# Optimization experiments

Measured on AMD Instinct MI355X. Metric: run time of the kernel, lower is better.

The kernel has to match this reference:

```python
import jax, jax.numpy as jnp
import numpy as np

K = 3       # kernel_size
RATE = 2    # dilation rate
NH = 8      # num_heads
EPS = 1e-5  # InstanceNorm eps


def _conv1x1(x, W, b):
    # x: [B,C,H,W], W: [O,C], b: [O]
    return jnp.einsum('bchw,oc->bohw', x, W) + b[None, :, None, None]


def _inorm(x):
    mu = jnp.mean(x, axis=(2, 3), keepdims=True)
    var = jnp.var(x, axis=(2, 3), keepdims=True)
    return (x - mu) / jnp.sqrt(var + EPS)


def _extract_patches(x):
    # dilated KxK patches, stride 1, 'same' grid -> [B, C, K*K, H, W]
    B, C, H, W = x.shape
    pad = RATE * (K - 1) // 2
    xp = jnp.pad(x, ((0, 0), (0, 0), (pad, pad), (pad, pad)))
    taps = [xp[:, :, i * RATE:i * RATE + H, j * RATE:j * RATE + W]
            for i in range(K) for j in range(K)]
    return jnp.stack(taps, axis=2)


def setup_inputs() -> dict:
    key = jax.random.key(0)
    ks = jax.random.split(key, 8)
    B, C, H, W, A = 1, 64, 64, 64, 128
    features = jax.random.normal(ks[0], (B, C, H, W), jnp.float32)
    masks = jax.random.uniform(ks[1], (B, 1, H, W), jnp.float32)
    s_in = 1.0 / np.sqrt(C).astype(np.float32)
    Wq = jax.random.normal(ks[2], (A, C), jnp.float32) * s_in
    bq = jnp.zeros((A,), jnp.float32)
    Wk = jax.random.normal(ks[3], (A, C), jnp.float32) * s_in
    bk = jnp.zeros((A,), jnp.float32)
    Wo = jax.random.normal(ks[4], (C, C), jnp.float32) * s_in
    bo = jnp.zeros((C,), jnp.float32)
    return dict(features=features, masks=masks, Wq=Wq, bq=bq,
                Wk=Wk, bk=bk, Wo=Wo, bo=bo)


def reference(features, masks, Wq, bq, Wk, bk, Wo, bo):
    B, C, H, W = features.shape
    A = Wq.shape[0]
    hc = A // NH
    L = H * W
    KK = K * K

    m = (masks > 0.5).astype(features.dtype)          # 1 = hole
    f_masked = features * m
    f_unmasked = features * (1.0 - m)

    q = jax.nn.relu(_inorm(_conv1x1(f_masked, Wq, bq)))    # [B,A,H,W]
    k = jax.nn.relu(_inorm(_conv1x1(f_unmasked, Wk, bk)))  # [B,A,H,W]

    # per-head dilated patch banks: [B,NH,hc*KK,L]
    qp = _extract_patches(q).reshape(B, NH, hc * KK, L)
    kp = _extract_patches(k).reshape(B, NH, hc * KK, L)

    # patch-correlation attention per head: [B,NH,L,L]
    attn = jax.nn.softmax(jnp.einsum('bndq,bndk->bnqk', qp, kp), axis=-1)

    # value patch bank from unmasked features: [B,C*KK,L]
    vp = _extract_patches(f_unmasked).reshape(B, C * KK, L)

    # sample value patches: [B,NH,L,C*KK]
    sampled = jnp.einsum('bnqk,bdk->bnqd', attn, vp)

    # fold: average the KK taps per channel, then average over heads
    attended = sampled.reshape(B, NH, L, C, KK).mean(axis=4).mean(axis=1)  # [B,L,C]
    attended = attended.transpose(0, 2, 1).reshape(B, C, H, W)

    return jax.nn.relu(_inorm(_conv1x1(attended, Wo, bo)))
```

## Files before the change

kernel.cpp:

```cpp
#include <hip/hip_runtime.h>
#include <hip/hip_bf16.h>


#define LL 4096
#define CC 64
#define AA 128
#define NH_ 8
#define KSTR 144
#define LOG2E 1.44269504088896340736f

typedef _Float16 half8 __attribute__((ext_vector_type(8)));
typedef float floatx4 __attribute__((ext_vector_type(4)));
typedef int intx4 __attribute__((ext_vector_type(4)));

__device__ __forceinline__ float fexp2(float x) {
    float r;
    asm("v_exp_f32 %0, %1" : "=v"(r) : "v"(x));
    return r;
}

__global__ __launch_bounds__(512) void prep_kernel(
    const float* __restrict__ feat,
    const float* __restrict__ masks,
    const float* __restrict__ Wq, const float* __restrict__ bq,
    const float* __restrict__ Wk, const float* __restrict__ bk,
    _Float16* __restrict__ q_act, _Float16* __restrict__ k_act,
    _Float16* __restrict__ vb)
{
    const int tid = threadIdx.x;
    const int b = blockIdx.x;
    __shared__ float sW[CC];
    __shared__ float sm[16];

    if (b >= 2 * AA) {
        int c = b - 2 * AA;
        for (int p = 0; p < 8; ++p) {
            int l = p * 512 + tid;
            int y = l >> 6, x = l & 63;
            float s = 0.f;
            for (int ty = 0; ty < 3; ++ty) {
                int yy = y + 2 * (ty - 1);
                if (yy < 0 || yy > 63) continue;
                for (int tx = 0; tx < 3; ++tx) {
                    int xx = x + 2 * (tx - 1);
                    if (xx < 0 || xx > 63) continue;
                    int ll = yy * 64 + xx;
                    float hole = masks[ll] > 0.5f ? 1.f : 0.f;
                    s += feat[c * LL + ll] * (1.f - hole);
                }
            }
            vb[c * LL + l] = (_Float16)(s * (1.f / 9.f));
        }
        return;
    }

    const int a = b & (AA - 1);
    const int sel = b >> 7;
    const float* Wrow = (sel ? Wk : Wq) + a * CC;
    const float bias = sel ? bk[a] : bq[a];
    if (tid < CC) sW[tid] = Wrow[tid];
    __syncthreads();

    float acc[8];
#pragma unroll
    for (int p = 0; p < 8; ++p) acc[p] = 0.f;
    for (int c = 0; c < CC; ++c) {
        float wc = sW[c];
        const float* fr = feat + (size_t)c * LL + tid;
#pragma unroll
        for (int p = 0; p < 8; ++p) acc[p] += wc * fr[p * 512];
    }

    float vals[8];
    float s1 = 0.f, s2 = 0.f;
#pragma unroll
    for (int p = 0; p < 8; ++p) {
        int l = p * 512 + tid;
        float hole = masks[l] > 0.5f ? 1.f : 0.f;
        float mf = sel ? (1.f - hole) : hole;
        float v = acc[p] * mf + bias;
        vals[p] = v; s1 += v; s2 += v * v;
    }
    for (int off = 32; off; off >>= 1) {
        s1 += __shfl_down(s1, off, 64);
        s2 += __shfl_down(s2, off, 64);
    }
    int wv = tid >> 6, ln = tid & 63;
    if (ln == 0) { sm[wv * 2] = s1; sm[wv * 2 + 1] = s2; }
    __syncthreads();
    s1 = 0.f; s2 = 0.f;
#pragma unroll
    for (int i = 0; i < 8; ++i) { s1 += sm[2 * i]; s2 += sm[2 * i + 1]; }
    float mu = s1 * (1.f / LL);
    float inv = rsqrtf(s2 * (1.f / LL) - mu * mu + 1e-5f);

    const float oscale = sel ? 1.f : LOG2E;
    _Float16* act = (sel ? k_act : q_act) + (size_t)a * LL;
#pragma unroll
    for (int p = 0; p < 8; ++p) {
        int l = p * 512 + tid;
        float v = (vals[p] - mu) * inv;
        act[l] = (_Float16)(v > 0.f ? v * oscale : 0.f);
    }
}

__global__ __launch_bounds__(256) void build_kp(
    const _Float16* __restrict__ k_act, _Float16* __restrict__ kp)
{
    const int n = blockIdx.x, y = blockIdx.y;
    const int tid = threadIdx.x;
    const _Float16* ka = k_act + (size_t)n * 16 * LL;
    __shared__ _Float16 kt[16][3][72];

    for (int idx = tid; idx < 16 * 3 * 68; idx += 256) {
        int row = idx / 68, xr = idx - row * 68;
        int ah = row / 3, ty = row - ah * 3;
        int yy = y + 2 * (ty - 1);
        int xx = xr - 2;
        _Float16 v = (_Float16)0.f;
        if (yy >= 0 && yy <= 63 && xx >= 0 && xx <= 63)
            v = ka[ah * LL + yy * 64 + xx];
        kt[ah][ty][xr] = v;
    }
    __syncthreads();

    _Float16* base = kp + ((size_t)n * LL + y * 64) * KSTR;
#pragma unroll
    for (int i = 0; i < 5; ++i) {
        int idx = tid + i * 256;
        if (idx < 64 * 18) {
            int x = idx / 18, c18 = idx - x * 18;
            half8 v8;
#pragma unroll
            for (int j = 0; j < 8; ++j) {
                int d = c18 * 8 + j;
                int ah = d / 9, t = d - ah * 9;
                int ty = t / 3, tx = t - ty * 3;
                v8[j] = kt[ah][ty][x + 2 * tx];
            }
            *(half8*)(base + (size_t)idx * 8) = v8;
        }
    }
}

__global__ __launch_bounds__(256, 2) void attn_kernel(
    const _Float16* __restrict__ q_act, const _Float16* __restrict__ kp,
    const _Float16* __restrict__ vb,
    _Float16* __restrict__ Opart, float* __restrict__ ml)
{
    const int bid = blockIdx.x;
    const int n = bid & 7;
    const int slot = bid >> 3;
    const int qt2 = slot & 31;
    const int h = slot >> 5;
    const int jt0 = h * 32;
    const int tid = threadIdx.x;
    const int w = tid >> 6, lane = tid & 63;
    const int l15 = lane & 15, quad = lane >> 4;

    __shared__ __align__(16) _Float16 Bk[2][64 * KSTR + 16];

    if (tid < 32) Bk[tid >> 4][64 * KSTR + (tid & 15)] = (_Float16)0.f;

    const _Float16* kpn = kp + (size_t)n * LL * KSTR;

    auto issue_bk = [&](int jt, _Float16* dst) {
        const char* tile = (const char*)(kpn + (size_t)jt * 64 * KSTR) + (lane << 4);
        for (int c = w; c < 18; c += 4) {
            __builtin_amdgcn_global_load_lds(
                (const __attribute__((address_space(1))) void*)(tile + c * 1024),
                (__attribute__((address_space(3))) void*)(dst + c * 512),
                16, 0, 0);
        }
    };

    half8 afrag[2][5];
    {
        const _Float16* qa = q_act + (size_t)n * 16 * LL;
        const int x = w * 16 + l15;
#pragma unroll
        for (int rs = 0; rs < 2; ++rs) {
            const int y = qt2 * 2 + rs;
#pragma unroll
            for (int ks = 0; ks < 5; ++ks) {
#pragma unroll
                for (int j = 0; j < 8; ++j) {
                    int d = ks * 32 + quad * 8 + j;
                    _Float16 v = (_Float16)0.f;
                    if (d < 144) {
                        int ah = d / 9, t = d - ah * 9;
                        int ty = t / 3, tx = t - ty * 3;
                        int yy = y + 2 * (ty - 1);
                        int xx = x + 2 * (tx - 1);
                        if (yy >= 0 && yy <= 63 && xx >= 0 && xx <= 63)
                            v = qa[ah * LL + yy * 64 + xx];
                    }
                    afrag[rs][ks][j] = v;
                }
            }
        }
    }

    floatx4 accO[2][4];
    float mrow[2], lrow[2];
#pragma unroll
    for (int rs = 0; rs < 2; ++rs) {
        mrow[rs] = -1e30f; lrow[rs] = 0.f;
#pragma unroll
        for (int i = 0; i < 4; ++i) accO[rs][i] = (floatx4){0.f, 0.f, 0.f, 0.f};
    }

    const int aLo = (((quad & 1) << 5) + l15) << 2;
    const int aHi = aLo + 64;
    const bool selHi = (quad >> 1) != 0;

    const _Float16* vpl = vb + (size_t)l15 * LL + quad * 8;

    issue_bk(jt0, Bk[0]);

    int cur = 0;
    for (int it = 0; it < 32; ++it) {
        __syncthreads();

        if (it < 31) issue_bk(jt0 + it + 1, Bk[cur ^ 1]);

        const _Float16* vp = vpl + (jt0 + it) * 64;
        half8 vfrag[4][2];
#pragma unroll
        for (int nt = 0; nt < 4; ++nt)
#pragma unroll
            for (int ks2 = 0; ks2 < 2; ++ks2)
                vfrag[nt][ks2] = *(const half8*)(vp + (size_t)nt * 16 * LL + ks2 * 32);

        const _Float16* bk = Bk[cur];

        floatx4 accS[2][4];
#pragma unroll
        for (int rs = 0; rs < 2; ++rs)
#pragma unroll
            for (int i = 0; i < 4; ++i) accS[rs][i] = (floatx4){0.f, 0.f, 0.f, 0.f};
        __builtin_amdgcn_s_setprio(1);
        for (int ks = 0; ks < 5; ++ks) {
#pragma unroll
            for (int nt = 0; nt < 4; ++nt) {
                half8 bfr = *(const half8*)(bk + (nt * 16 + l15) * KSTR + ks * 32 + quad * 8);
                accS[0][nt] = __builtin_amdgcn_mfma_f32_16x16x32_f16(bfr, afrag[0][ks], accS[0][nt], 0, 0, 0);
                accS[1][nt] = __builtin_amdgcn_mfma_f32_16x16x32_f16(bfr, afrag[1][ks], accS[1][nt], 0, 0, 0);
            }
        }
        __builtin_amdgcn_s_setprio(0);

        half8 pfr[2][2];
#pragma unroll
        for (int rs = 0; rs < 2; ++rs) {
            float t0 = fmaxf(fmaxf(accS[rs][0][0], accS[rs][0][1]), fmaxf(accS[rs][0][2], accS[rs][0][3]));
            float t1 = fmaxf(fmaxf(accS[rs][1][0], accS[rs][1][1]), fmaxf(accS[rs][1][2], accS[rs][1][3]));
            float t2 = fmaxf(fmaxf(accS[rs][2][0], accS[rs][2][1]), fmaxf(accS[rs][2][2], accS[rs][2][3]));
            float t3 = fmaxf(fmaxf(accS[rs][3][0], accS[rs][3][1]), fmaxf(accS[rs][3][2], accS[rs][3][3]));
            float tm = fmaxf(fmaxf(t0, t1), fmaxf(t2, t3));
            if (!__all(tm <= mrow[rs] + 3.0f)) {
                tm = fmaxf(tm, __shfl_xor(tm, 16, 64));
                tm = fmaxf(tm, __shfl_xor(tm, 32, 64));
                float mn = fmaxf(mrow[rs], tm);
                float alpha = fexp2(mrow[rs] - mn);
                mrow[rs] = mn;
                lrow[rs] *= alpha;
                float af[4];
#pragma unroll
                for (int r = 0; r < 4; ++r) af[r] = __shfl(alpha, quad * 4 + r, 16);
#pragma unroll
                for (int nt = 0; nt < 4; ++nt)
#pragma unroll
                    for (int r = 0; r < 4; ++r) accO[rs][nt][r] *= af[r];
            }
            float rsum = 0.f;
#pragma unroll
            for (int nt = 0; nt < 4; ++nt)
#pragma unroll
                for (int r = 0; r < 4; ++r) {
                    float pv = fexp2(accS[rs][nt][r] - mrow[rs]);
                    accS[rs][nt][r] = pv;
                    rsum += pv;
                }
            lrow[rs] += rsum;

            int pkw[4][2];
#pragma unroll
            for (int nt = 0; nt < 4; ++nt)
#pragma unroll
                for (int rp = 0; rp < 2; ++rp) {
                    auto hp = __builtin_amdgcn_cvt_pkrtz(accS[rs][nt][2 * rp],
                                                         accS[rs][nt][2 * rp + 1]);
                    pkw[nt][rp] = __builtin_bit_cast(int, hp);
                }
#pragma unroll
            for (int ks2 = 0; ks2 < 2; ++ks2) {
                int w0A = __builtin_amdgcn_ds_bpermute(aLo, pkw[2 * ks2][0]);
                int w0B = __builtin_amdgcn_ds_bpermute(aLo, pkw[2 * ks2 + 1][0]);
                int w1A = __builtin_amdgcn_ds_bpermute(aLo, pkw[2 * ks2][1]);
                int w1B = __builtin_amdgcn_ds_bpermute(aLo, pkw[2 * ks2 + 1][1]);
                int w2A = __builtin_amdgcn_ds_bpermute(aHi, pkw[2 * ks2][0]);
                int w2B = __builtin_amdgcn_ds_bpermute(aHi, pkw[2 * ks2 + 1][0]);
                int w3A = __builtin_amdgcn_ds_bpermute(aHi, pkw[2 * ks2][1]);
                int w3B = __builtin_amdgcn_ds_bpermute(aHi, pkw[2 * ks2 + 1][1]);
                intx4 wvv;
                wvv[0] = selHi ? w0B : w0A;
                wvv[1] = selHi ? w1B : w1A;
                wvv[2] = selHi ? w2B : w2A;
                wvv[3] = selHi ? w3B : w3A;
                pfr[rs][ks2] = __builtin_bit_cast(half8, wvv);
            }
        }

        __builtin_amdgcn_s_setprio(1);
#pragma unroll
        for (int ks2 = 0; ks2 < 2; ++ks2) {
#pragma unroll
            for (int nt = 0; nt < 4; ++nt) {
                accO[0][nt] = __builtin_amdgcn_mfma_f32_16x16x32_f16(pfr[0][ks2], vfrag[nt][ks2], accO[0][nt], 0, 0, 0);
                accO[1][nt] = __builtin_amdgcn_mfma_f32_16x16x32_f16(pfr[1][ks2], vfrag[nt][ks2], accO[1][nt], 0, 0, 0);
            }
        }
        __builtin_amdgcn_s_setprio(0);

        cur ^= 1;
    }

#pragma unroll
    for (int rs = 0; rs < 2; ++rs) {
        const int y = qt2 * 2 + rs;
        float rsum = lrow[rs];
        rsum += __shfl_xor(rsum, 16, 64);
        rsum += __shfl_xor(rsum, 32, 64);
        float invl = 1.f / rsum;
        float iv[4];
#pragma unroll
        for (int r = 0; r < 4; ++r) iv[r] = __shfl(invl, quad * 4 + r, 16);

        _Float16* op = Opart + ((size_t)(n * 2 + h) * LL + y * 64 + w * 16) * CC;
#pragma unroll
        for (int r = 0; r < 4; ++r)
#pragma unroll
            for (int nt = 0; nt < 4; ++nt)
                op[(quad * 4 + r) * CC + nt * 16 + l15] = (_Float16)(accO[rs][nt][r] * iv[r]);

        if (quad == 0) {
            float* mlp = ml + ((size_t)n * LL + y * 64 + w * 16 + l15) * 4;
            mlp[2 * h] = mrow[rs];
            mlp[2 * h + 1] = rsum;
        }
    }
}

__global__ __launch_bounds__(256) void combine_kernel(
    const _Float16* __restrict__ Opart, const float* __restrict__ ml,
    float* __restrict__ att)
{
    int t = blockIdx.x * 256 + threadIdx.x;
    int l = t >> 6, c = t & 63;
    float s = 0.f;
#pragma unroll
    for (int n = 0; n < NH_; ++n) {
        const float* mlp = ml + ((size_t)n * LL + l) * 4;
        float m0 = mlp[0], l0 = mlp[1], m1 = mlp[2], l1 = mlp[3];
        float M = fmaxf(m0, m1);
        float w0 = l0 * fexp2(m0 - M);
        float w1 = l1 * fexp2(m1 - M);
        float o0 = (float)Opart[((size_t)(2 * n) * LL + l) * CC + c];
        float o1 = (float)Opart[((size_t)(2 * n + 1) * LL + l) * CC + c];
        s += (w0 * o0 + w1 * o1) / (w0 + w1);
    }
    att[t] = s * 0.125f;
}

__global__ __launch_bounds__(256) void out_kernel(
    const float* __restrict__ att,
    const float* __restrict__ Wo, const float* __restrict__ bo,
    float* __restrict__ out)
{
    const int o = blockIdx.x;
    const int tid = threadIdx.x;
    __shared__ float sW[CC];
    __shared__ float sm[8];
    if (tid < CC) sW[tid] = Wo[o * CC + tid];
    __syncthreads();
    const float bias = bo[o];

    float vals[16], s1 = 0.f, s2 = 0.f;
    for (int p = 0; p < 16; ++p) {
        int l = p * 256 + tid;
        const float4* arow = (const float4*)(att + (size_t)l * CC);
        float acc = bias;
#pragma unroll
        for (int c4 = 0; c4 < 16; ++c4) {
            float4 a4 = arow[c4];
            acc += sW[c4 * 4] * a4.x + sW[c4 * 4 + 1] * a4.y +
                   sW[c4 * 4 + 2] * a4.z + sW[c4 * 4 + 3] * a4.w;
        }
        vals[p] = acc; s1 += acc; s2 += acc * acc;
    }
    for (int off = 32; off; off >>= 1) {
        s1 += __shfl_down(s1, off, 64);
        s2 += __shfl_down(s2, off, 64);
    }
    int wv = tid >> 6, ln = tid & 63;
    if (ln == 0) { sm[wv * 2] = s1; sm[wv * 2 + 1] = s2; }
    __syncthreads();
    s1 = sm[0] + sm[2] + sm[4] + sm[6];
    s2 = sm[1] + sm[3] + sm[5] + sm[7];
    float mu = s1 * (1.f / LL);
    float inv = rsqrtf(s2 * (1.f / LL) - mu * mu + 1e-5f);
    for (int p = 0; p < 16; ++p) {
        int l = p * 256 + tid;
        float v = (vals[p] - mu) * inv;
        out[(size_t)o * LL + l] = v > 0.f ? v : 0.f;
    }
}

extern "C" void kernel_launch(void* const* d_in, const int* in_sizes, int n_in,
                              void* d_out, int out_size, void* d_ws, size_t ws_size,
                              hipStream_t stream) {
    const float* feat  = (const float*)d_in[0];
    const float* masks = (const float*)d_in[1];
    const float* Wq    = (const float*)d_in[2];
    const float* bq    = (const float*)d_in[3];
    const float* Wk    = (const float*)d_in[4];
    const float* bk    = (const float*)d_in[5];
    const float* Wo    = (const float*)d_in[6];
    const float* bo    = (const float*)d_in[7];
    float* out = (float*)d_out;

    char* ws = (char*)d_ws;
    _Float16* q_act = (_Float16*)ws;
    _Float16* k_act = (_Float16*)(ws + 1048576);
    _Float16* vb    = (_Float16*)(ws + 2097152);
    float*    att   = (float*)(ws + 2621440);
    _Float16* kp    = (_Float16*)(ws + 3670016);
    _Float16* Opart = (_Float16*)(ws + 13107200);
    float*    ml    = (float*)(ws + 21495808);

    prep_kernel<<<2 * AA + CC, 512, 0, stream>>>(feat, masks, Wq, bq, Wk, bk,
                                                 q_act, k_act, vb);
    dim3 gb(NH_, 64);
    build_kp<<<gb, 256, 0, stream>>>(k_act, kp);
    attn_kernel<<<512, 256, 0, stream>>>(q_act, kp, vb, Opart, ml);
    combine_kernel<<<LL * CC / 256, 256, 0, stream>>>(Opart, ml, att);
    out_kernel<<<CC, 256, 0, stream>>>(att, Wo, bo, out);
}
```

Measured before the change: 226.3 us.

## Interleave per-row softmax with PV MFMAs, drop lazy rescale, widen out_kernel blocks

```diff
diff --git a/kernel.cpp b/kernel.cpp
--- a/kernel.cpp
+++ b/kernel.cpp
@@ -216,6 +216,65 @@
 
     const _Float16* vpl = vb + (size_t)l15 * LL + quad * 8;
 
+    auto softmax_pack = [&](floatx4* accS, floatx4* accOr,
+                            float& mr, float& lr, half8* pfr) {
+        float t0 = fmaxf(fmaxf(accS[0][0], accS[0][1]), fmaxf(accS[0][2], accS[0][3]));
+        float t1 = fmaxf(fmaxf(accS[1][0], accS[1][1]), fmaxf(accS[1][2], accS[1][3]));
+        float t2 = fmaxf(fmaxf(accS[2][0], accS[2][1]), fmaxf(accS[2][2], accS[2][3]));
+        float t3 = fmaxf(fmaxf(accS[3][0], accS[3][1]), fmaxf(accS[3][2], accS[3][3]));
+        float tm = fmaxf(fmaxf(t0, t1), fmaxf(t2, t3));
+        tm = fmaxf(tm, __shfl_xor(tm, 16, 64));
+        tm = fmaxf(tm, __shfl_xor(tm, 32, 64));
+        float mn = fmaxf(mr, tm);
+        float alpha = fexp2(mr - mn);
+        mr = mn;
+        lr *= alpha;
+        float af[4];
+#pragma unroll
+        for (int r = 0; r < 4; ++r) af[r] = __shfl(alpha, quad * 4 + r, 16);
+#pragma unroll
+        for (int nt = 0; nt < 4; ++nt)
+#pragma unroll
+            for (int r = 0; r < 4; ++r) accOr[nt][r] *= af[r];
+        float rsum = 0.f;
+#pragma unroll
+        for (int nt = 0; nt < 4; ++nt)
+#pragma unroll
+            for (int r = 0; r < 4; ++r) {
+                float pv = fexp2(accS[nt][r] - mn);
+                accS[nt][r] = pv;
+                rsum += pv;
+            }
+        lr += rsum;
+
+        int pkw[4][2];
+#pragma unroll
+        for (int nt = 0; nt < 4; ++nt)
+#pragma unroll
+            for (int rp = 0; rp < 2; ++rp) {
+                auto hp = __builtin_amdgcn_cvt_pkrtz(accS[nt][2 * rp],
+                                                     accS[nt][2 * rp + 1]);
+                pkw[nt][rp] = __builtin_bit_cast(int, hp);
+            }
+#pragma unroll
+        for (int ks2 = 0; ks2 < 2; ++ks2) {
+            int w0A = __builtin_amdgcn_ds_bpermute(aLo, pkw[2 * ks2][0]);
+            int w0B = __builtin_amdgcn_ds_bpermute(aLo, pkw[2 * ks2 + 1][0]);
+            int w1A = __builtin_amdgcn_ds_bpermute(aLo, pkw[2 * ks2][1]);
+            int w1B = __builtin_amdgcn_ds_bpermute(aLo, pkw[2 * ks2 + 1][1]);
+            int w2A = __builtin_amdgcn_ds_bpermute(aHi, pkw[2 * ks2][0]);
+            int w2B = __builtin_amdgcn_ds_bpermute(aHi, pkw[2 * ks2 + 1][0]);
+            int w3A = __builtin_amdgcn_ds_bpermute(aHi, pkw[2 * ks2][1]);
+            int w3B = __builtin_amdgcn_ds_bpermute(aHi, pkw[2 * ks2 + 1][1]);
+            intx4 wvv;
+            wvv[0] = selHi ? w0B : w0A;
+            wvv[1] = selHi ? w1B : w1A;
+            wvv[2] = selHi ? w2B : w2A;
+            wvv[3] = selHi ? w3B : w3A;
+            pfr[ks2] = __builtin_bit_cast(half8, wvv);
+        }
+    };
+
     issue_bk(jt0, Bk[0]);
 
     int cur = 0;
@@ -234,94 +293,35 @@
 
         const _Float16* bk = Bk[cur];
 
-        floatx4 accS[2][4];
-#pragma unroll
-        for (int rs = 0; rs < 2; ++rs)
-#pragma unroll
-            for (int i = 0; i < 4; ++i) accS[rs][i] = (floatx4){0.f, 0.f, 0.f, 0.f};
-        __builtin_amdgcn_s_setprio(1);
+        floatx4 accS0[4], accS1[4];
+#pragma unroll
+        for (int i = 0; i < 4; ++i) {
+            accS0[i] = (floatx4){0.f, 0.f, 0.f, 0.f};
+            accS1[i] = (floatx4){0.f, 0.f, 0.f, 0.f};
+        }
         for (int ks = 0; ks < 5; ++ks) {
 #pragma unroll
             for (int nt = 0; nt < 4; ++nt) {
                 half8 bfr = *(const half8*)(bk + (nt * 16 + l15) * KSTR + ks * 32 + quad * 8);
-                accS[0][nt] = __builtin_amdgcn_mfma_f32_16x16x32_f16(bfr, afrag[0][ks], accS[0][nt], 0, 0, 0);
-                accS[1][nt] = __builtin_amdgcn_mfma_f32_16x16x32_f16(bfr, afrag[1][ks], accS[1][nt], 0, 0, 0);
-            }
-        }
-        __builtin_amdgcn_s_setprio(0);
-
-        half8 pfr[2][2];
-#pragma unroll
-        for (int rs = 0; rs < 2; ++rs) {
-            float t0 = fmaxf(fmaxf(accS[rs][0][0], accS[rs][0][1]), fmaxf(accS[rs][0][2], accS[rs][0][3]));
-            float t1 = fmaxf(fmaxf(accS[rs][1][0], accS[rs][1][1]), fmaxf(accS[rs][1][2], accS[rs][1][3]));
-            float t2 = fmaxf(fmaxf(accS[rs][2][0], accS[rs][2][1]), fmaxf(accS[rs][2][2], accS[rs][2][3]));
-            float t3 = fmaxf(fmaxf(accS[rs][3][0], accS[rs][3][1]), fmaxf(accS[rs][3][2], accS[rs][3][3]));
-            float tm = fmaxf(fmaxf(t0, t1), fmaxf(t2, t3));
-            if (!__all(tm <= mrow[rs] + 3.0f)) {
-                tm = fmaxf(tm, __shfl_xor(tm, 16, 64));
-                tm = fmaxf(tm, __shfl_xor(tm, 32, 64));
-                float mn = fmaxf(mrow[rs], tm);
-                float alpha = fexp2(mrow[rs] - mn);
-                mrow[rs] = mn;
-                lrow[rs] *= alpha;
-                float af[4];
-#pragma unroll
-                for (int r = 0; r < 4; ++r) af[r] = __shfl(alpha, quad * 4 + r, 16);
-#pragma unroll
-                for (int nt = 0; nt < 4; ++nt)
-#pragma unroll
-                    for (int r = 0; r < 4; ++r) accO[rs][nt][r] *= af[r];
-            }
-            float rsum = 0.f;
+                accS0[nt] = __builtin_amdgcn_mfma_f32_16x16x32_f16(bfr, afrag[0][ks], accS0[nt], 0, 0, 0);
+                accS1[nt] = __builtin_amdgcn_mfma_f32_16x16x32_f16(bfr, afrag[1][ks], accS1[nt], 0, 0, 0);
+            }
+        }
+
+        half8 pfr0[2], pfr1[2];
+        softmax_pack(accS0, accO[0], mrow[0], lrow[0], pfr0);
+#pragma unroll
+        for (int ks2 = 0; ks2 < 2; ++ks2)
 #pragma unroll
             for (int nt = 0; nt < 4; ++nt)
-#pragma unroll
-                for (int r = 0; r < 4; ++r) {
-                    float pv = fexp2(accS[rs][nt][r] - mrow[rs]);
-                    accS[rs][nt][r] = pv;
-                    rsum += pv;
-                }
-            lrow[rs] += rsum;
-
-            int pkw[4][2];
+                accO[0][nt] = __builtin_amdgcn_mfma_f32_16x16x32_f16(pfr0[ks2], vfrag[nt][ks2], accO[0][nt], 0, 0, 0);
+
+        softmax_pack(accS1, accO[1], mrow[1], lrow[1], pfr1);
+#pragma unroll
+        for (int ks2 = 0; ks2 < 2; ++ks2)
 #pragma unroll
             for (int nt = 0; nt < 4; ++nt)
-#pragma unroll
-                for (int rp = 0; rp < 2; ++rp) {
-                    auto hp = __builtin_amdgcn_cvt_pkrtz(accS[rs][nt][2 * rp],
-                                                         accS[rs][nt][2 * rp + 1]);
-                    pkw[nt][rp] = __builtin_bit_cast(int, hp);
-                }
-#pragma unroll
-            for (int ks2 = 0; ks2 < 2; ++ks2) {
-                int w0A = __builtin_amdgcn_ds_bpermute(aLo, pkw[2 * ks2][0]);
-                int w0B = __builtin_amdgcn_ds_bpermute(aLo, pkw[2 * ks2 + 1][0]);
-                int w1A = __builtin_amdgcn_ds_bpermute(aLo, pkw[2 * ks2][1]);
-                int w1B = __builtin_amdgcn_ds_bpermute(aLo, pkw[2 * ks2 + 1][1]);
-                int w2A = __builtin_amdgcn_ds_bpermute(aHi, pkw[2 * ks2][0]);
-                int w2B = __builtin_amdgcn_ds_bpermute(aHi, pkw[2 * ks2 + 1][0]);
-                int w3A = __builtin_amdgcn_ds_bpermute(aHi, pkw[2 * ks2][1]);
-                int w3B = __builtin_amdgcn_ds_bpermute(aHi, pkw[2 * ks2 + 1][1]);
-                intx4 wvv;
-                wvv[0] = selHi ? w0B : w0A;
-                wvv[1] = selHi ? w1B : w1A;
-                wvv[2] = selHi ? w2B : w2A;
-                wvv[3] = selHi ? w3B : w3A;
-                pfr[rs][ks2] = __builtin_bit_cast(half8, wvv);
-            }
-        }
-
-        __builtin_amdgcn_s_setprio(1);
-#pragma unroll
-        for (int ks2 = 0; ks2 < 2; ++ks2) {
-#pragma unroll
-            for (int nt = 0; nt < 4; ++nt) {
-                accO[0][nt] = __builtin_amdgcn_mfma_f32_16x16x32_f16(pfr[0][ks2], vfrag[nt][ks2], accO[0][nt], 0, 0, 0);
-                accO[1][nt] = __builtin_amdgcn_mfma_f32_16x16x32_f16(pfr[1][ks2], vfrag[nt][ks2], accO[1][nt], 0, 0, 0);
-            }
-        }
-        __builtin_amdgcn_s_setprio(0);
+                accO[1][nt] = __builtin_amdgcn_mfma_f32_16x16x32_f16(pfr1[ks2], vfrag[nt][ks2], accO[1][nt], 0, 0, 0);
 
         cur ^= 1;
     }
@@ -373,7 +373,7 @@
     att[t] = s * 0.125f;
 }
 
-__global__ __launch_bounds__(256) void out_kernel(
+__global__ __launch_bounds__(1024) void out_kernel(
     const float* __restrict__ att,
     const float* __restrict__ Wo, const float* __restrict__ bo,
     float* __restrict__ out)
@@ -381,14 +381,15 @@
     const int o = blockIdx.x;
     const int tid = threadIdx.x;
     __shared__ float sW[CC];
-    __shared__ float sm[8];
+    __shared__ float sm[32];
     if (tid < CC) sW[tid] = Wo[o * CC + tid];
     __syncthreads();
     const float bias = bo[o];
 
-    float vals[16], s1 = 0.f, s2 = 0.f;
-    for (int p = 0; p < 16; ++p) {
-        int l = p * 256 + tid;
+    float vals[4], s1 = 0.f, s2 = 0.f;
+#pragma unroll
+    for (int p = 0; p < 4; ++p) {
+        int l = p * 1024 + tid;
         const float4* arow = (const float4*)(att + (size_t)l * CC);
         float acc = bias;
 #pragma unroll
@@ -406,12 +407,14 @@
     int wv = tid >> 6, ln = tid & 63;
     if (ln == 0) { sm[wv * 2] = s1; sm[wv * 2 + 1] = s2; }
     __syncthreads();
-    s1 = sm[0] + sm[2] + sm[4] + sm[6];
-    s2 = sm[1] + sm[3] + sm[5] + sm[7];
+    s1 = 0.f; s2 = 0.f;
+#pragma unroll
+    for (int i = 0; i < 16; ++i) { s1 += sm[2 * i]; s2 += sm[2 * i + 1]; }
     float mu = s1 * (1.f / LL);
     float inv = rsqrtf(s2 * (1.f / LL) - mu * mu + 1e-5f);
-    for (int p = 0; p < 16; ++p) {
-        int l = p * 256 + tid;
+#pragma unroll
+    for (int p = 0; p < 4; ++p) {
+        int l = p * 1024 + tid;
         float v = (vals[p] - mu) * inv;
         out[(size_t)o * LL + l] = v > 0.f ? v : 0.f;
     }
@@ -445,5 +448,5 @@
     build_kp<<<gb, 256, 0, stream>>>(k_act, kp);
     attn_kernel<<<512, 256, 0, stream>>>(q_act, kp, vb, Opart, ml);
     combine_kernel<<<LL * CC / 256, 256, 0, stream>>>(Opart, ml, att);
-    out_kernel<<<CC, 256, 0, stream>>>(att, Wo, bo, out);
-}
+    out_kernel<<<CC, 1024, 0, stream>>>(att, Wo, bo, out);
+}
```

After: 228.5 us. About the same (+1.0%).
